# Kernel optimization log

Measured on AMD Instinct MI355X. Metric: run time of the kernel, lower is better.

## Reference

```python
import jax, jax.numpy as jnp
import numpy as np

B, S, D = 8, 1024, 1024

def setup_inputs() -> dict:
    key = jax.random.key(0)
    k1, k2, k3, k4, k5 = jax.random.split(key, 5)
    head = jax.random.normal(k1, (B, S, D), dtype=jnp.float32)
    dep = jax.random.normal(k2, (B, S, D), dtype=jnp.float32)
    edge_U = jax.random.normal(k3, (D, D), dtype=jnp.float32) * (1.0 / np.sqrt(D))
    edge_W = jax.random.normal(k4, (1, 2 * D), dtype=jnp.float32) * (1.0 / np.sqrt(2 * D))
    edge_b = jax.random.normal(k5, (1,), dtype=jnp.float32)
    return {"head": head, "dep": dep, "edge_U": edge_U, "edge_W": edge_W, "edge_b": edge_b}

def reference(head, dep, edge_U, edge_W, edge_b):
    # t1[b,i,j] = head[b,i,:] @ edge_U @ dep[b,j,:]
    t1 = jnp.einsum('bid,dk,bjk->bij', head, edge_U, dep)
    # t2: original concatenates [head_i ; dep_j] for every (i,j) pair and applies
    # edge_W [1, 2D]. Algebraically t2[b,i,j] = head_i @ W[:D] + dep_j @ W[D:],
    # so we compute two [B,S] projections and broadcast-add (same math, no
    # O(B*S^2*2D) intermediate).
    d = head.shape[-1]
    w = edge_W[0]
    s_head = head @ w[:d]   # [B, S]
    s_dep = dep @ w[d:]     # [B, S]
    return t1 + s_head[:, :, None] + s_dep[:, None, :] + edge_b[0]
```

## Files before the change

kernel.cpp:

```cpp
#include <hip/hip_runtime.h>
#include <hip/hip_bf16.h>
#include <stdint.h>

#define D_DIM 1024
#define B_DIM 8
#define S_DIM 1024

typedef __bf16 bf16;
typedef __bf16 bf16x4 __attribute__((ext_vector_type(4)));
typedef __bf16 bf16x8 __attribute__((ext_vector_type(8)));
typedef float floatx4 __attribute__((ext_vector_type(4)));

__device__ __forceinline__ void async_copy16(const void* g, void* l) {
    __builtin_amdgcn_global_load_lds(
        (const __attribute__((address_space(1))) void*)g,
        (__attribute__((address_space(3))) void*)l, 16, 0, 0);
}

__global__ __launch_bounds__(256) void prep_kernel(
    const float* __restrict__ head, const float* __restrict__ dep,
    const float* __restrict__ U, const float* __restrict__ edge_W,
    bf16* __restrict__ head_b, bf16* __restrict__ dep_b,
    bf16* __restrict__ U_b,
    float* __restrict__ s_head, float* __restrict__ s_dep)
{
    int blk  = blockIdx.x;
    int wid  = threadIdx.x >> 6;
    int lane = threadIdx.x & 63;

    if (blk < 4096) {
        int row = blk * 4 + wid;

        const float* src;
        bf16* dst;
        const float* w;
        float* sout;
        if (row < B_DIM * S_DIM) {
            src  = head   + (size_t)row * D_DIM;
            dst  = head_b + (size_t)row * D_DIM;
            w    = edge_W;
            sout = s_head + row;
        } else {
            int r = row - B_DIM * S_DIM;
            src  = dep   + (size_t)r * D_DIM;
            dst  = dep_b + (size_t)r * D_DIM;
            w    = edge_W + D_DIM;
            sout = s_dep + r;
        }
        float d = 0.0f;
        #pragma unroll
        for (int it = 0; it < 4; ++it) {
            int idx = it * 64 + lane;
            float4 v  = ((const float4*)src)[idx];
            float4 wv = ((const float4*)w)[idx];
            bf16x4 o;
            o[0] = (bf16)v.x; o[1] = (bf16)v.y; o[2] = (bf16)v.z; o[3] = (bf16)v.w;
            ((bf16x4*)dst)[idx] = o;
            d += v.x * wv.x + v.y * wv.y + v.z * wv.z + v.w * wv.w;
        }
        #pragma unroll
        for (int off = 32; off > 0; off >>= 1)
            d += __shfl_down(d, off, 64);
        if (lane == 0) *sout = d;
    } else {
        int row = (blk - 4096) * 4 + wid;
        const float* src = U   + (size_t)row * D_DIM;
        bf16*        dst = U_b + (size_t)row * D_DIM;
        #pragma unroll
        for (int it = 0; it < 4; ++it) {
            int idx = it * 64 + lane;
            float4 v = ((const float4*)src)[idx];
            bf16x4 o;
            o[0] = (bf16)v.x; o[1] = (bf16)v.y; o[2] = (bf16)v.z; o[3] = (bf16)v.w;
            ((bf16x4*)dst)[idx] = o;
        }
    }
}

template <int EPI>
__global__ __launch_bounds__(512, 4) void gemm_bt_kernel(
    const bf16* __restrict__ A, const bf16* __restrict__ Bt,
    void* __restrict__ Cout,
    int N,
    long long sA, long long sB, long long sC,
    const float* __restrict__ s_row, const float* __restrict__ s_col,
    const float* __restrict__ bias)
{
    const int BK = 64;
    __shared__ bf16 As[128 * BK];
    __shared__ bf16 Bs[128 * BK];

    int tid  = threadIdx.x;
    int wid  = tid >> 6;
    int lane = tid & 63;
    int quad = lane >> 4;
    int l16  = lane & 15;
    int wr   = wid >> 2;
    int wc   = wid & 3;

    int nx  = gridDim.x, ny = gridDim.y;
    int lin = blockIdx.x + nx * (blockIdx.y + ny * blockIdx.z);
    int nwg = nx * ny * gridDim.z;
    int swz = (lin & 7) * (nwg >> 3) + (lin >> 3);
    int bx  = swz % nx;
    int rem = swz / nx;
    int by  = rem % ny;
    int bz  = rem / ny;

    int tile_m = by * 128;
    int tile_n = bx * 128;

    const bf16* Ab = A  + (size_t)bz * sA + (size_t)tile_m * D_DIM;
    const bf16* Bb = Bt + (size_t)bz * sB + (size_t)tile_n * D_DIM;

    floatx4 zero = {0.0f, 0.0f, 0.0f, 0.0f};
    floatx4 acc[4][2];
    #pragma unroll
    for (int i = 0; i < 4; ++i)
        #pragma unroll
        for (int j = 0; j < 2; ++j) acc[i][j] = zero;

    for (int k0 = 0; k0 < D_DIM; k0 += BK) {
        #pragma unroll
        for (int it = 0; it < 2; ++it) {
            int g  = wid * 128 + it * 64 + lane;
            int r  = g >> 3;
            int cg = (g & 7) ^ (r & 7);
            int ldsoff = (wid * 128 + it * 64) * 8;
            async_copy16(Ab + (size_t)r * D_DIM + k0 + cg * 8, &As[ldsoff]);
            async_copy16(Bb + (size_t)r * D_DIM + k0 + cg * 8, &Bs[ldsoff]);
        }
        __syncthreads();

        #pragma unroll
        for (int kk = 0; kk < BK; kk += 32) {
            bf16x8 a[4], b[2];
            #pragma unroll
            for (int mt = 0; mt < 4; ++mt) {
                int row  = wr * 64 + mt * 16 + l16;
                int slot = ((kk >> 3) + quad) ^ (row & 7);
                a[mt] = *(const bf16x8*)&As[row * BK + slot * 8];
            }
            #pragma unroll
            for (int nt = 0; nt < 2; ++nt) {
                int row  = wc * 32 + nt * 16 + l16;
                int slot = ((kk >> 3) + quad) ^ (row & 7);
                b[nt] = *(const bf16x8*)&Bs[row * BK + slot * 8];
            }
            #pragma unroll
            for (int mt = 0; mt < 4; ++mt)
                #pragma unroll
                for (int nt = 0; nt < 2; ++nt)
                    acc[mt][nt] = __builtin_amdgcn_mfma_f32_16x16x32_bf16(
                        a[mt], b[nt], acc[mt][nt], 0, 0, 0);
        }
        __syncthreads();
    }

    int row0 = tile_m + wr * 64;
    int col0 = tile_n + wc * 32;
    if (EPI == 0) {
        bf16* Cb = (bf16*)Cout + (size_t)bz * sC;
        #pragma unroll
        for (int mt = 0; mt < 4; ++mt)
            #pragma unroll
            for (int r = 0; r < 4; ++r) {
                int row = row0 + mt * 16 + quad * 4 + r;
                #pragma unroll
                for (int nt = 0; nt < 2; ++nt) {
                    int col = col0 + nt * 16 + l16;
                    Cb[(size_t)row * N + col] = (bf16)acc[mt][nt][r];
                }
            }
    } else {
        float* Cf = (float*)Cout + (size_t)bz * sC;
        float b0 = bias[0];
        const float* srow = s_row + (size_t)bz * S_DIM;
        const float* scol = s_col + (size_t)bz * S_DIM;
        #pragma unroll
        for (int mt = 0; mt < 4; ++mt)
            #pragma unroll
            for (int r = 0; r < 4; ++r) {
                int row = row0 + mt * 16 + quad * 4 + r;
                float sh = srow[row] + b0;
                #pragma unroll
                for (int nt = 0; nt < 2; ++nt) {
                    int col = col0 + nt * 16 + l16;
                    __builtin_nontemporal_store(acc[mt][nt][r] + sh + scol[col],
                                                &Cf[(size_t)row * N + col]);
                }
            }
    }
}

extern "C" void kernel_launch(void* const* d_in, const int* in_sizes, int n_in,
                              void* d_out, int out_size, void* d_ws, size_t ws_size,
                              hipStream_t stream) {
    const float* head   = (const float*)d_in[0];
    const float* dep    = (const float*)d_in[1];
    const float* edge_U = (const float*)d_in[2];
    const float* edge_W = (const float*)d_in[3];
    const float* edge_b = (const float*)d_in[4];
    float* out = (float*)d_out;

    char* ws = (char*)d_ws;
    const size_t nBSD = (size_t)B_DIM * S_DIM * D_DIM;

    bf16*  head_b = (bf16*)ws;  ws += nBSD * sizeof(bf16);
    bf16*  dep_b  = (bf16*)ws;  ws += nBSD * sizeof(bf16);
    bf16*  U_b    = (bf16*)ws;  ws += (size_t)D_DIM * D_DIM * sizeof(bf16);
    bf16*  tmpD   = (bf16*)ws;  ws += nBSD * sizeof(bf16);
    float* s_head = (float*)ws; ws += (size_t)B_DIM * S_DIM * sizeof(float);
    float* s_dep  = (float*)ws; ws += (size_t)B_DIM * S_DIM * sizeof(float);

    prep_kernel<<<4096 + 256, 256, 0, stream>>>(
        head, dep, edge_U, edge_W, head_b, dep_b, U_b, s_head, s_dep);

    gemm_bt_kernel<0><<<dim3(D_DIM / 128, (B_DIM * S_DIM) / 128, 1), 512, 0, stream>>>(
        dep_b, U_b, tmpD, D_DIM,
        0, 0, 0, nullptr, nullptr, nullptr);

    gemm_bt_kernel<1><<<dim3(S_DIM / 128, S_DIM / 128, B_DIM), 512, 0, stream>>>(
        head_b, tmpD, out, S_DIM,
        (long long)S_DIM * D_DIM, (long long)S_DIM * D_DIM,
        (long long)S_DIM * S_DIM,
        s_head, s_dep, edge_b);
}
```

Before: 156.5 us.

## Fuse both GEMMs into one persistent kernel with a grid-wide atomic barrier

Merges the dep·U GEMM and the batched head·tmpD GEMM into a single 512-block launch. A global atomic counter acts as a grid barrier between the two phases, which removes one kernel launch and its tail. It also adds s_setprio around the MFMA blocks. The barrier relies on all 512 blocks being co-resident, since with launch bounds of 512 threads and 4 blocks per CU there are enough CUs; a spin-wait plus an extra memset launch are the costs.

```diff
diff --git a/kernel.cpp b/kernel.cpp
--- a/kernel.cpp
+++ b/kernel.cpp
@@ -77,18 +77,60 @@
     }
 }
 
-template <int EPI>
-__global__ __launch_bounds__(512, 4) void gemm_bt_kernel(
-    const bf16* __restrict__ A, const bf16* __restrict__ Bt,
-    void* __restrict__ Cout,
-    int N,
-    long long sA, long long sB, long long sC,
-    const float* __restrict__ s_row, const float* __restrict__ s_col,
-    const float* __restrict__ bias)
+__device__ __forceinline__ void gemm_core(
+    const bf16* __restrict__ Ab, const bf16* __restrict__ Bb,
+    bf16* As, bf16* Bs, floatx4 (&acc)[4][2],
+    int wid, int lane, int quad, int l16, int wr, int wc)
 {
-    const int BK = 64;
-    __shared__ bf16 As[128 * BK];
-    __shared__ bf16 Bs[128 * BK];
+    for (int k0 = 0; k0 < D_DIM; k0 += 64) {
+        #pragma unroll
+        for (int it = 0; it < 2; ++it) {
+            int g  = wid * 128 + it * 64 + lane;
+            int r  = g >> 3;
+            int cg = (g & 7) ^ (r & 7);
+            int ldsoff = (wid * 128 + it * 64) * 8;
+            async_copy16(Ab + (size_t)r * D_DIM + k0 + cg * 8, &As[ldsoff]);
+            async_copy16(Bb + (size_t)r * D_DIM + k0 + cg * 8, &Bs[ldsoff]);
+        }
+        __syncthreads();
+
+        #pragma unroll
+        for (int kk = 0; kk < 64; kk += 32) {
+            bf16x8 a[4], b[2];
+            #pragma unroll
+            for (int mt = 0; mt < 4; ++mt) {
+                int row  = wr * 64 + mt * 16 + l16;
+                int slot = ((kk >> 3) + quad) ^ (row & 7);
+                a[mt] = *(const bf16x8*)&As[row * 64 + slot * 8];
+            }
+            #pragma unroll
+            for (int nt = 0; nt < 2; ++nt) {
+                int row  = wc * 32 + nt * 16 + l16;
+                int slot = ((kk >> 3) + quad) ^ (row & 7);
+                b[nt] = *(const bf16x8*)&Bs[row * 64 + slot * 8];
+            }
+            __builtin_amdgcn_s_setprio(1);
+            #pragma unroll
+            for (int mt = 0; mt < 4; ++mt)
+                #pragma unroll
+                for (int nt = 0; nt < 2; ++nt)
+                    acc[mt][nt] = __builtin_amdgcn_mfma_f32_16x16x32_bf16(
+                        a[mt], b[nt], acc[mt][nt], 0, 0, 0);
+            __builtin_amdgcn_s_setprio(0);
+        }
+        __syncthreads();
+    }
+}
+
+__global__ __launch_bounds__(512, 4) void gemm_fused(
+    const bf16* __restrict__ dep_b, const bf16* __restrict__ U_b,
+    const bf16* __restrict__ head_b,
+    bf16* __restrict__ tmpD, float* __restrict__ out,
+    const float* __restrict__ s_head, const float* __restrict__ s_dep,
+    const float* __restrict__ edge_b, int* __restrict__ bar)
+{
+    __shared__ bf16 As[128 * 64];
+    __shared__ bf16 Bs[128 * 64];
 
     int tid  = threadIdx.x;
     int wid  = tid >> 6;
@@ -98,69 +140,28 @@
     int wr   = wid >> 2;
     int wc   = wid & 3;
 
-    int nx  = gridDim.x, ny = gridDim.y;
-    int lin = blockIdx.x + nx * (blockIdx.y + ny * blockIdx.z);
-    int nwg = nx * ny * gridDim.z;
-    int swz = (lin & 7) * (nwg >> 3) + (lin >> 3);
-    int bx  = swz % nx;
-    int rem = swz / nx;
-    int by  = rem % ny;
-    int bz  = rem / ny;
-
-    int tile_m = by * 128;
-    int tile_n = bx * 128;
-
-    const bf16* Ab = A  + (size_t)bz * sA + (size_t)tile_m * D_DIM;
-    const bf16* Bb = Bt + (size_t)bz * sB + (size_t)tile_n * D_DIM;
-
-    floatx4 zero = {0.0f, 0.0f, 0.0f, 0.0f};
-    floatx4 acc[4][2];
-    #pragma unroll
-    for (int i = 0; i < 4; ++i)
-        #pragma unroll
-        for (int j = 0; j < 2; ++j) acc[i][j] = zero;
-
-    for (int k0 = 0; k0 < D_DIM; k0 += BK) {
-        #pragma unroll
-        for (int it = 0; it < 2; ++it) {
-            int g  = wid * 128 + it * 64 + lane;
-            int r  = g >> 3;
-            int cg = (g & 7) ^ (r & 7);
-            int ldsoff = (wid * 128 + it * 64) * 8;
-            async_copy16(Ab + (size_t)r * D_DIM + k0 + cg * 8, &As[ldsoff]);
-            async_copy16(Bb + (size_t)r * D_DIM + k0 + cg * 8, &Bs[ldsoff]);
-        }
-        __syncthreads();
-
-        #pragma unroll
-        for (int kk = 0; kk < BK; kk += 32) {
-            bf16x8 a[4], b[2];
-            #pragma unroll
-            for (int mt = 0; mt < 4; ++mt) {
-                int row  = wr * 64 + mt * 16 + l16;
-                int slot = ((kk >> 3) + quad) ^ (row & 7);
-                a[mt] = *(const bf16x8*)&As[row * BK + slot * 8];
-            }
-            #pragma unroll
-            for (int nt = 0; nt < 2; ++nt) {
-                int row  = wc * 32 + nt * 16 + l16;
-                int slot = ((kk >> 3) + quad) ^ (row & 7);
-                b[nt] = *(const bf16x8*)&Bs[row * BK + slot * 8];
-            }
-            #pragma unroll
-            for (int mt = 0; mt < 4; ++mt)
-                #pragma unroll
-                for (int nt = 0; nt < 2; ++nt)
-                    acc[mt][nt] = __builtin_amdgcn_mfma_f32_16x16x32_bf16(
-                        a[mt], b[nt], acc[mt][nt], 0, 0, 0);
-        }
-        __syncthreads();
-    }
-
-    int row0 = tile_m + wr * 64;
-    int col0 = tile_n + wc * 32;
-    if (EPI == 0) {
-        bf16* Cb = (bf16*)Cout + (size_t)bz * sC;
+    int lin = blockIdx.x;
+    int swz = (lin & 7) * 64 + (lin >> 3);
+
+    {
+        int bx = swz & 7;
+        int by = swz >> 3;
+        int tile_m = by * 128;
+        int tile_n = bx * 128;
+        const bf16* Ab = dep_b + (size_t)tile_m * D_DIM;
+        const bf16* Bb = U_b   + (size_t)tile_n * D_DIM;
+
+        floatx4 zero = {0.0f, 0.0f, 0.0f, 0.0f};
+        floatx4 acc[4][2];
+        #pragma unroll
+        for (int i = 0; i < 4; ++i)
+            #pragma unroll
+            for (int j = 0; j < 2; ++j) acc[i][j] = zero;
+
+        gemm_core(Ab, Bb, As, Bs, acc, wid, lane, quad, l16, wr, wc);
+
+        int row0 = tile_m + wr * 64;
+        int col0 = tile_n + wc * 32;
         #pragma unroll
         for (int mt = 0; mt < 4; ++mt)
             #pragma unroll
@@ -169,14 +170,45 @@
                 #pragma unroll
                 for (int nt = 0; nt < 2; ++nt) {
                     int col = col0 + nt * 16 + l16;
-                    Cb[(size_t)row * N + col] = (bf16)acc[mt][nt][r];
+                    tmpD[(size_t)row * D_DIM + col] = (bf16)acc[mt][nt][r];
                 }
             }
-    } else {
-        float* Cf = (float*)Cout + (size_t)bz * sC;
-        float b0 = bias[0];
-        const float* srow = s_row + (size_t)bz * S_DIM;
-        const float* scol = s_col + (size_t)bz * S_DIM;
+    }
+
+    __syncthreads();
+    if (tid == 0) {
+        __threadfence();
+        atomicAdd(bar, 1);
+        while (atomicAdd(bar, 0) < 512)
+            __builtin_amdgcn_s_sleep(8);
+        __threadfence();
+    }
+    __syncthreads();
+
+    {
+        int bx = swz & 7;
+        int by = (swz >> 3) & 7;
+        int bz = swz >> 6;
+        int tile_m = by * 128;
+        int tile_n = bx * 128;
+        const bf16* Ab = head_b + (size_t)bz * S_DIM * D_DIM + (size_t)tile_m * D_DIM;
+        const bf16* Bb = tmpD   + (size_t)bz * S_DIM * D_DIM + (size_t)tile_n * D_DIM;
+
+        floatx4 zero = {0.0f, 0.0f, 0.0f, 0.0f};
+        floatx4 acc[4][2];
+        #pragma unroll
+        for (int i = 0; i < 4; ++i)
+            #pragma unroll
+            for (int j = 0; j < 2; ++j) acc[i][j] = zero;
+
+        gemm_core(Ab, Bb, As, Bs, acc, wid, lane, quad, l16, wr, wc);
+
+        float b0 = edge_b[0];
+        const float* srow = s_head + (size_t)bz * S_DIM;
+        const float* scol = s_dep  + (size_t)bz * S_DIM;
+        float* Cf = out + (size_t)bz * S_DIM * S_DIM;
+        int row0 = tile_m + wr * 64;
+        int col0 = tile_n + wc * 32;
         #pragma unroll
         for (int mt = 0; mt < 4; ++mt)
             #pragma unroll
@@ -187,7 +219,7 @@
                 for (int nt = 0; nt < 2; ++nt) {
                     int col = col0 + nt * 16 + l16;
                     __builtin_nontemporal_store(acc[mt][nt][r] + sh + scol[col],
-                                                &Cf[(size_t)row * N + col]);
+                                                &Cf[(size_t)row * S_DIM + col]);
                 }
             }
     }
@@ -212,17 +244,13 @@
     bf16*  tmpD   = (bf16*)ws;  ws += nBSD * sizeof(bf16);
     float* s_head = (float*)ws; ws += (size_t)B_DIM * S_DIM * sizeof(float);
     float* s_dep  = (float*)ws; ws += (size_t)B_DIM * S_DIM * sizeof(float);
+    int*   bar    = (int*)ws;   ws += 16;
+
+    hipMemsetAsync(bar, 0, sizeof(int), stream);
 
     prep_kernel<<<4096 + 256, 256, 0, stream>>>(
         head, dep, edge_U, edge_W, head_b, dep_b, U_b, s_head, s_dep);
 
-    gemm_bt_kernel<0><<<dim3(D_DIM / 128, (B_DIM * S_DIM) / 128, 1), 512, 0, stream>>>(
-        dep_b, U_b, tmpD, D_DIM,
-        0, 0, 0, nullptr, nullptr, nullptr);
-
-    gemm_bt_kernel<1><<<dim3(S_DIM / 128, S_DIM / 128, B_DIM), 512, 0, stream>>>(
-        head_b, tmpD, out, S_DIM,
-        (long long)S_DIM * D_DIM, (long long)S_DIM * D_DIM,
-        (long long)S_DIM * S_DIM,
-        s_head, s_dep, edge_b);
-}
+    gemm_fused<<<512, 512, 0, stream>>>(
+        dep_b, U_b, head_b, tmpD, out, s_head, s_dep, edge_b, bar);
+}
```

New measurement: 221.5 us. +41.5%, slower.
